# Kernel optimization log

Hardware: AMD Instinct MI355X
Metric: run time of the kernel (lower is better)

Reference implementation:

```python
import jax, jax.numpy as jnp
import numpy as np

H = 8   # no_heads
D = 32  # c_hidden per head


def setup_inputs() -> dict:
    key = jax.random.key(0)
    ks = jax.random.split(key, 8)
    B, Q, K, C = 4, 1024, 1024, 256
    s = 0.02
    return {
        "q_x": jax.random.normal(ks[0], (B, Q, C), jnp.float32),
        "kv_x": jax.random.normal(ks[1], (B, K, C), jnp.float32),
        "mask_bias": jnp.zeros((B, 1, 1, K), jnp.float32),
        "pair_bias": jax.random.normal(ks[2], (B, H, Q, K), jnp.float32),
        "wq": jax.random.normal(ks[3], (H * D, C), jnp.float32) * s,
        "wk": jax.random.normal(ks[4], (H * D, C), jnp.float32) * s,
        "wv": jax.random.normal(ks[5], (H * D, C), jnp.float32) * s,
        "wg": jax.random.normal(ks[6], (H * D, C), jnp.float32) * s,
        "bg": jnp.zeros((H * D,), jnp.float32),
        "wo": jax.random.normal(ks[7], (C, H * D), jnp.float32) * s,
        "bo": jnp.zeros((C,), jnp.float32),
    }


def reference(q_x, kv_x, mask_bias, pair_bias, wq, wk, wv, wg, bg, wo, bo):
    B, Q, _ = q_x.shape
    K = kv_x.shape[1]
    # linear projections (no bias on q/k/v, as in OpenFold Attention)
    q = (q_x @ wq.T).reshape(B, Q, H, D) / jnp.sqrt(jnp.asarray(D, q_x.dtype))
    k = (kv_x @ wk.T).reshape(B, K, H, D)
    v = (kv_x @ wv.T).reshape(B, K, H, D)
    # scores + biases (mask bias broadcasts over heads/queries)
    a = jnp.einsum("bqhd,bkhd->bhqk", q, k) + mask_bias + pair_bias
    a = jax.nn.softmax(a, axis=-1)
    o = jnp.einsum("bhqk,bkhd->bqhd", a, v)  # [B,Q,H,D]
    # multiplicative gating from the query input
    g = jax.nn.sigmoid(q_x @ wg.T + bg).reshape(B, Q, H, D)
    o = o * g
    return (o.reshape(B, Q, H * D)) @ wo.T + bo
```

## Files before the change

### kernel.cpp

```cpp
#include <hip/hip_runtime.h>
#include <cstdint>
#include <cstddef>

typedef short bf16x8 __attribute__((ext_vector_type(8)));
typedef float f32x4 __attribute__((ext_vector_type(4)));
typedef unsigned short u16x4 __attribute__((ext_vector_type(4)));
typedef unsigned short u16x8 __attribute__((ext_vector_type(8)));

#define MFMA(a,b,c) __builtin_amdgcn_mfma_f32_16x16x32_bf16((a),(b),(c),0,0,0)

__device__ __forceinline__ unsigned short f2bf(float x){
  union { float f; unsigned u; } v; v.f = x;
  unsigned r = v.u + 0x7FFFu + ((v.u >> 16) & 1u);
  return (unsigned short)(r >> 16);
}
__device__ __forceinline__ float bf2f(unsigned short b){
  union { unsigned u; float f; } v; v.u = ((unsigned)b) << 16;
  return v.f;
}
__device__ __forceinline__ bf16x8 cvtld8(const float* p){
  f32x4 a = *(const f32x4*)p;
  f32x4 b = *(const f32x4*)(p + 4);
  bf16x8 r;
  r[0]=(short)f2bf(a.x); r[1]=(short)f2bf(a.y);
  r[2]=(short)f2bf(a.z); r[3]=(short)f2bf(a.w);
  r[4]=(short)f2bf(b.x); r[5]=(short)f2bf(b.y);
  r[6]=(short)f2bf(b.z); r[7]=(short)f2bf(b.w);
  return r;
}

__global__ __launch_bounds__(256) void wcvt_kernel(
    const float* __restrict__ wq, const float* __restrict__ wk,
    const float* __restrict__ wv, const float* __restrict__ wg,
    const float* __restrict__ wo, unsigned short* __restrict__ dst)
{
  const int which = blockIdx.x >> 5;
  const float* s = (which==0)?wq:(which==1)?wk:(which==2)?wv:(which==3)?wg:wo;
  const int off = (blockIdx.x & 31) * 2048 + threadIdx.x * 8;
  f32x4 a = *(const f32x4*)(s + off);
  f32x4 b = *(const f32x4*)(s + off + 4);
  u16x8 r;
  r[0]=f2bf(a.x); r[1]=f2bf(a.y); r[2]=f2bf(a.z); r[3]=f2bf(a.w);
  r[4]=f2bf(b.x); r[5]=f2bf(b.y); r[6]=f2bf(b.z); r[7]=f2bf(b.w);
  *(u16x8*)(dst + (size_t)which*65536 + off) = r;
}

__global__ __launch_bounds__(256,2) void proj_kernel(
    const float* __restrict__ q_x, const float* __restrict__ kv_x,
    const unsigned short* __restrict__ wb,
    const float* __restrict__ bg,
    unsigned short* __restrict__ qws, unsigned short* __restrict__ kws,
    unsigned short* __restrict__ vTws, unsigned short* __restrict__ gws)
{
  const int tid = threadIdx.x;
  const int w = tid >> 6, lane = tid & 63;
  const int c = lane & 15, qd = lane >> 4;
  const int side = blockIdx.x >> 8;
  const int rb = (blockIdx.x & 255) * 16;
  const float* X = side ? kv_x : q_x;
  const unsigned short* W0 = wb + (size_t)(side ? 1 : 0) * 65536;
  const unsigned short* W1 = wb + (size_t)(side ? 2 : 3) * 65536;
  const int hdw = w * 64;

  const f32x4 fz = {0.f,0.f,0.f,0.f};
  f32x4 acc[2][4];
  #pragma unroll
  for (int o=0;o<2;o++)
    #pragma unroll
    for (int mt=0;mt<4;mt++) acc[o][mt] = fz;

  #pragma unroll
  for (int ks = 0; ks < 8; ks++){
    const int ko = ks*32 + qd*8;
    bf16x8 bfrag = cvtld8(X + (size_t)(rb + c)*256 + ko);
    #pragma unroll
    for (int mt = 0; mt < 4; mt++){
      const int hd = hdw + mt*16 + c;
      bf16x8 a0 = *(const bf16x8*)(W0 + (size_t)hd*256 + ko);
      bf16x8 a1 = *(const bf16x8*)(W1 + (size_t)hd*256 + ko);
      acc[0][mt] = MFMA(a0, bfrag, acc[0][mt]);
      acc[1][mt] = MFMA(a1, bfrag, acc[1][mt]);
    }
  }

  const int row = rb + c;
  const int b = row >> 10, rr = row & 1023;
  #pragma unroll
  for (int mt = 0; mt < 4; mt++){
    const int hd0 = hdw + mt*16 + qd*4;
    const int h = hd0 >> 5, d0 = hd0 & 31;
    f32x4 v0 = acc[0][mt], v1 = acc[1][mt];
    if (side == 0){
      const float qs = 0.17677669529663687f;
      u16x4 oq = { f2bf(v0.x*qs), f2bf(v0.y*qs), f2bf(v0.z*qs), f2bf(v0.w*qs) };
      *(u16x4*)(qws + ((size_t)((b*8 + h)*1024 + rr))*32 + d0) = oq;
      f32x4 bg4 = *(const f32x4*)(bg + hd0);
      float g0 = 1.f/(1.f + exp2f(-1.44269504f*(v1.x + bg4.x)));
      float g1 = 1.f/(1.f + exp2f(-1.44269504f*(v1.y + bg4.y)));
      float g2 = 1.f/(1.f + exp2f(-1.44269504f*(v1.z + bg4.z)));
      float g3 = 1.f/(1.f + exp2f(-1.44269504f*(v1.w + bg4.w)));
      u16x4 og = { f2bf(g0), f2bf(g1), f2bf(g2), f2bf(g3) };
      *(u16x4*)(gws + ((size_t)((b*1024 + rr)*8 + h))*32 + d0) = og;
    } else {
      u16x4 ok = { f2bf(v0.x), f2bf(v0.y), f2bf(v0.z), f2bf(v0.w) };
      *(u16x4*)(kws + ((size_t)((b*8 + h)*1024 + rr))*32 + d0) = ok;
      size_t vb = ((size_t)((b*8 + h)*32 + d0))*1024 + rr;
      vTws[vb         ] = f2bf(v1.x);
      vTws[vb + 1024  ] = f2bf(v1.y);
      vTws[vb + 2048  ] = f2bf(v1.z);
      vTws[vb + 3072  ] = f2bf(v1.w);
    }
  }
}

__global__ __launch_bounds__(256,4) void attn_kernel(
    const float* __restrict__ pair_bias, const float* __restrict__ mask_bias,
    const unsigned short* __restrict__ qws, const unsigned short* __restrict__ kws,
    const unsigned short* __restrict__ vTws, const unsigned short* __restrict__ gws,
    unsigned short* __restrict__ ows)
{
  __shared__ __align__(16) unsigned short pT[4*16*136];

  const int tid = threadIdx.x;
  const int w = tid >> 6, lane = tid & 63;
  const int c = lane & 15, qd = lane >> 4;
  const int bh = blockIdx.x >> 4, qb = blockIdx.x & 15;
  const int b  = bh >> 3, h = bh & 7;
  const int qrow = qb*64 + w*16 + c;

  const bf16x8 qf = *(const bf16x8*)(qws + ((size_t)bh*1024 + qrow)*32 + qd*8);
  const float* pbp = pair_bias + ((size_t)bh*1024 + qrow)*1024;
  const float* mbp = mask_bias + (size_t)b*1024;
  const unsigned short* kbase = kws  + (size_t)bh*1024*32;
  const unsigned short* vbase = vTws + (size_t)bh*32*1024;
  unsigned short* pTw = pT + w*(16*136);

  const f32x4 fz = {0.f,0.f,0.f,0.f};
  float m_i = -3.0e38f, l_i = 0.f;
  f32x4 accO0 = fz, accO1 = fz;

  for (int kc = 0; kc < 8; kc++){
    const int k0 = kc*128;
    f32x4 sf[8];
    float cmax = -3.0e38f;
    #pragma unroll
    for (int t = 0; t < 8; t++){
      const int kt = k0 + t*16;
      bf16x8 af = *(const bf16x8*)(kbase + (size_t)(kt + c)*32 + qd*8);
      f32x4 s = MFMA(af, qf, fz);
      f32x4 pb = *(const f32x4*)(pbp + kt + qd*4);
      f32x4 mb = *(const f32x4*)(mbp + kt + qd*4);
      s = (s + pb + mb) * 1.44269504f;
      sf[t] = s;
      cmax = fmaxf(cmax, fmaxf(fmaxf(s.x, s.y), fmaxf(s.z, s.w)));
    }
    cmax = fmaxf(cmax, __shfl_xor(cmax, 16));
    cmax = fmaxf(cmax, __shfl_xor(cmax, 32));
    const float m_new = fmaxf(m_i, cmax);
    const float alpha = exp2f(m_i - m_new);
    accO0 *= alpha; accO1 *= alpha;

    float rsum = 0.f;
    #pragma unroll
    for (int t = 0; t < 8; t++){
      f32x4 p;
      p.x = exp2f(sf[t].x - m_new);
      p.y = exp2f(sf[t].y - m_new);
      p.z = exp2f(sf[t].z - m_new);
      p.w = exp2f(sf[t].w - m_new);
      rsum += (p.x + p.y) + (p.z + p.w);
      u16x4 pk = { f2bf(p.x), f2bf(p.y), f2bf(p.z), f2bf(p.w) };
      *(u16x4*)(pTw + c*136 + t*16 + qd*4) = pk;
    }
    rsum += __shfl_xor(rsum, 16);
    rsum += __shfl_xor(rsum, 32);
    l_i = l_i*alpha + rsum;
    m_i = m_new;

    #pragma unroll
    for (int ks = 0; ks < 4; ks++){
      bf16x8 pf = *(const bf16x8*)(pTw + c*136 + ks*32 + qd*8);
      bf16x8 v0 = *(const bf16x8*)(vbase + (size_t)c*1024      + k0 + ks*32 + qd*8);
      bf16x8 v1 = *(const bf16x8*)(vbase + (size_t)(16+c)*1024 + k0 + ks*32 + qd*8);
      accO0 = MFMA(v0, pf, accO0);
      accO1 = MFMA(v1, pf, accO1);
    }
  }

  const float inv_l = 1.0f / l_i;
  const size_t obase = (((size_t)b*1024 + qrow)*8 + h)*32;
  {
    u16x4 g4 = *(const u16x4*)(gws + obase + qd*4);
    u16x4 o4 = { f2bf(accO0.x*inv_l*bf2f(g4[0])),
                 f2bf(accO0.y*inv_l*bf2f(g4[1])),
                 f2bf(accO0.z*inv_l*bf2f(g4[2])),
                 f2bf(accO0.w*inv_l*bf2f(g4[3])) };
    *(u16x4*)(ows + obase + qd*4) = o4;
  }
  {
    u16x4 g4 = *(const u16x4*)(gws + obase + 16 + qd*4);
    u16x4 o4 = { f2bf(accO1.x*inv_l*bf2f(g4[0])),
                 f2bf(accO1.y*inv_l*bf2f(g4[1])),
                 f2bf(accO1.z*inv_l*bf2f(g4[2])),
                 f2bf(accO1.w*inv_l*bf2f(g4[3])) };
    *(u16x4*)(ows + obase + 16 + qd*4) = o4;
  }
}

__global__ __launch_bounds__(256,2) void oproj_kernel(
    const unsigned short* __restrict__ ows, const unsigned short* __restrict__ wob,
    const float* __restrict__ bo, float* __restrict__ out)
{
  const int tid = threadIdx.x;
  const int w = tid >> 6, lane = tid & 63;
  const int c = lane & 15, qd = lane >> 4;
  const int row0 = blockIdx.x * 16;
  const int i0 = w * 64;

  const f32x4 fz = {0.f,0.f,0.f,0.f};
  f32x4 acc[4] = {fz, fz, fz, fz};
  #pragma unroll
  for (int ks = 0; ks < 8; ks++){
    const int ko = ks*32 + qd*8;
    bf16x8 bfrag = *(const bf16x8*)(ows + (size_t)(row0 + c)*256 + ko);
    #pragma unroll
    for (int mt = 0; mt < 4; mt++){
      bf16x8 afrag = *(const bf16x8*)(wob + (size_t)(i0 + mt*16 + c)*256 + ko);
      acc[mt] = MFMA(afrag, bfrag, acc[mt]);
    }
  }
  #pragma unroll
  for (int mt = 0; mt < 4; mt++){
    const int i = i0 + mt*16 + qd*4;
    f32x4 bo4 = *(const f32x4*)(bo + i);
    f32x4 r = acc[mt] + bo4;
    *(f32x4*)(out + (size_t)(row0 + c)*256 + i) = r;
  }
}

extern "C" void kernel_launch(void* const* d_in, const int* in_sizes, int n_in,
                              void* d_out, int out_size, void* d_ws, size_t ws_size,
                              hipStream_t stream) {
  const float* q_x       = (const float*)d_in[0];
  const float* kv_x      = (const float*)d_in[1];
  const float* mask_bias = (const float*)d_in[2];
  const float* pair_bias = (const float*)d_in[3];
  const float* wq        = (const float*)d_in[4];
  const float* wk        = (const float*)d_in[5];
  const float* wv        = (const float*)d_in[6];
  const float* wg        = (const float*)d_in[7];
  const float* bg        = (const float*)d_in[8];
  const float* wo        = (const float*)d_in[9];
  const float* bo        = (const float*)d_in[10];

  unsigned short* ws  = (unsigned short*)d_ws;
  unsigned short* qws  = ws;
  unsigned short* kws  = ws + (1u<<20);
  unsigned short* vTws = ws + 2*(1u<<20);
  unsigned short* gws  = ws + 3*(1u<<20);
  unsigned short* ows  = ws + 4*(1u<<20);
  unsigned short* wb   = ws + 5*(1u<<20);

  wcvt_kernel<<<160, 256, 0, stream>>>(wq, wk, wv, wg, wo, wb);
  proj_kernel<<<512, 256, 0, stream>>>(q_x, kv_x, wb, bg, qws, kws, vTws, gws);
  attn_kernel<<<512, 256, 0, stream>>>(pair_bias, mask_bias, qws, kws, vTws, gws, ows);
  oproj_kernel<<<256, 256, 0, stream>>>(ows, wb + 4*65536, bo, (float*)d_out);
}
```

Baseline: 268.5 us.

## Software-pipeline pair_bias and K loads across key chunks in attention kernel

```diff
diff --git a/kernel.cpp b/kernel.cpp
--- a/kernel.cpp
+++ b/kernel.cpp
@@ -113,7 +113,7 @@
   }
 }
 
-__global__ __launch_bounds__(256,4) void attn_kernel(
+__global__ __launch_bounds__(256,2) void attn_kernel(
     const float* __restrict__ pair_bias, const float* __restrict__ mask_bias,
     const unsigned short* __restrict__ qws, const unsigned short* __restrict__ kws,
     const unsigned short* __restrict__ vTws, const unsigned short* __restrict__ gws,
@@ -139,20 +139,45 @@
   float m_i = -3.0e38f, l_i = 0.f;
   f32x4 accO0 = fz, accO1 = fz;
 
+  f32x4 pb0[8], pb1[8];
+  bf16x8 afb[8];
+  #pragma unroll
+  for (int t = 0; t < 8; t++)
+    pb0[t] = *(const f32x4*)(pbp + t*16 + qd*4);
+  #pragma unroll
+  for (int t = 0; t < 8; t++)
+    pb1[t] = *(const f32x4*)(pbp + 128 + t*16 + qd*4);
+  #pragma unroll
+  for (int t = 0; t < 8; t++)
+    afb[t] = *(const bf16x8*)(kbase + (size_t)(t*16 + c)*32 + qd*8);
+
+  #pragma unroll
   for (int kc = 0; kc < 8; kc++){
     const int k0 = kc*128;
     f32x4 sf[8];
+    #pragma unroll
+    for (int t = 0; t < 8; t++)
+      sf[t] = MFMA(afb[t], qf, fz);
+    if (kc < 7){
+      #pragma unroll
+      for (int t = 0; t < 8; t++)
+        afb[t] = *(const bf16x8*)(kbase + (size_t)(k0 + 128 + t*16 + c)*32 + qd*8);
+    }
     float cmax = -3.0e38f;
     #pragma unroll
     for (int t = 0; t < 8; t++){
-      const int kt = k0 + t*16;
-      bf16x8 af = *(const bf16x8*)(kbase + (size_t)(kt + c)*32 + qd*8);
-      f32x4 s = MFMA(af, qf, fz);
-      f32x4 pb = *(const f32x4*)(pbp + kt + qd*4);
-      f32x4 mb = *(const f32x4*)(mbp + kt + qd*4);
-      s = (s + pb + mb) * 1.44269504f;
+      f32x4 mb = *(const f32x4*)(mbp + k0 + t*16 + qd*4);
+      f32x4 pb = (kc & 1) ? pb1[t] : pb0[t];
+      f32x4 s = (sf[t] + pb + mb) * 1.44269504f;
       sf[t] = s;
       cmax = fmaxf(cmax, fmaxf(fmaxf(s.x, s.y), fmaxf(s.z, s.w)));
+    }
+    if (kc < 6){
+      #pragma unroll
+      for (int t = 0; t < 8; t++){
+        f32x4 v = *(const f32x4*)(pbp + k0 + 256 + t*16 + qd*4);
+        if (kc & 1) pb1[t] = v; else pb0[t] = v;
+      }
     }
     cmax = fmaxf(cmax, __shfl_xor(cmax, 16));
     cmax = fmaxf(cmax, __shfl_xor(cmax, 32));
```

Result: slower. 285.5 us (+6.3%).

## Split attention over key halves and add a combine kernel; prefetch K and pair bias

Applied to the files above, without the earlier changes.

```diff
diff --git a/kernel.cpp b/kernel.cpp
--- a/kernel.cpp
+++ b/kernel.cpp
@@ -116,43 +116,59 @@
 __global__ __launch_bounds__(256,4) void attn_kernel(
     const float* __restrict__ pair_bias, const float* __restrict__ mask_bias,
     const unsigned short* __restrict__ qws, const unsigned short* __restrict__ kws,
-    const unsigned short* __restrict__ vTws, const unsigned short* __restrict__ gws,
-    unsigned short* __restrict__ ows)
+    const unsigned short* __restrict__ vTws,
+    float* __restrict__ pO, float* __restrict__ pML)
 {
   __shared__ __align__(16) unsigned short pT[4*16*136];
 
   const int tid = threadIdx.x;
   const int w = tid >> 6, lane = tid & 63;
   const int c = lane & 15, qd = lane >> 4;
-  const int bh = blockIdx.x >> 4, qb = blockIdx.x & 15;
-  const int b  = bh >> 3, h = bh & 7;
+  const int split = blockIdx.x >> 9;
+  const int rblk  = blockIdx.x & 511;
+  const int bh = rblk >> 4, qb = rblk & 15;
+  const int b  = bh >> 3;
   const int qrow = qb*64 + w*16 + c;
+  const int kbeg = split*512;
 
   const bf16x8 qf = *(const bf16x8*)(qws + ((size_t)bh*1024 + qrow)*32 + qd*8);
-  const float* pbp = pair_bias + ((size_t)bh*1024 + qrow)*1024;
-  const float* mbp = mask_bias + (size_t)b*1024;
-  const unsigned short* kbase = kws  + (size_t)bh*1024*32;
-  const unsigned short* vbase = vTws + (size_t)bh*32*1024;
+  const float* pbp = pair_bias + ((size_t)bh*1024 + qrow)*1024 + kbeg;
+  const float* mbp = mask_bias + (size_t)b*1024 + kbeg;
+  const unsigned short* kbase = kws  + ((size_t)bh*1024 + kbeg)*32;
+  const unsigned short* vbase = vTws + (size_t)bh*32*1024 + kbeg;
   unsigned short* pTw = pT + w*(16*136);
 
   const f32x4 fz = {0.f,0.f,0.f,0.f};
   float m_i = -3.0e38f, l_i = 0.f;
   f32x4 accO0 = fz, accO1 = fz;
 
-  for (int kc = 0; kc < 8; kc++){
+  bf16x8 afb[8];
+  f32x4  pbb[8];
+  #pragma unroll
+  for (int t = 0; t < 8; t++){
+    afb[t] = *(const bf16x8*)(kbase + (size_t)(t*16 + c)*32 + qd*8);
+    pbb[t] = *(const f32x4*)(pbp + t*16 + qd*4);
+  }
+
+  #pragma unroll
+  for (int kc = 0; kc < 4; kc++){
     const int k0 = kc*128;
     f32x4 sf[8];
     float cmax = -3.0e38f;
     #pragma unroll
     for (int t = 0; t < 8; t++){
-      const int kt = k0 + t*16;
-      bf16x8 af = *(const bf16x8*)(kbase + (size_t)(kt + c)*32 + qd*8);
-      f32x4 s = MFMA(af, qf, fz);
-      f32x4 pb = *(const f32x4*)(pbp + kt + qd*4);
-      f32x4 mb = *(const f32x4*)(mbp + kt + qd*4);
-      s = (s + pb + mb) * 1.44269504f;
+      f32x4 s = MFMA(afb[t], qf, fz);
+      f32x4 mb = *(const f32x4*)(mbp + k0 + t*16 + qd*4);
+      s = (s + pbb[t] + mb) * 1.44269504f;
       sf[t] = s;
       cmax = fmaxf(cmax, fmaxf(fmaxf(s.x, s.y), fmaxf(s.z, s.w)));
+    }
+    if (kc < 3){
+      #pragma unroll
+      for (int t = 0; t < 8; t++){
+        afb[t] = *(const bf16x8*)(kbase + (size_t)(k0 + 128 + t*16 + c)*32 + qd*8);
+        pbb[t] = *(const f32x4*)(pbp + k0 + 128 + t*16 + qd*4);
+      }
     }
     cmax = fmaxf(cmax, __shfl_xor(cmax, 16));
     cmax = fmaxf(cmax, __shfl_xor(cmax, 32));
@@ -187,24 +203,47 @@
     }
   }
 
-  const float inv_l = 1.0f / l_i;
-  const size_t obase = (((size_t)b*1024 + qrow)*8 + h)*32;
-  {
-    u16x4 g4 = *(const u16x4*)(gws + obase + qd*4);
-    u16x4 o4 = { f2bf(accO0.x*inv_l*bf2f(g4[0])),
-                 f2bf(accO0.y*inv_l*bf2f(g4[1])),
-                 f2bf(accO0.z*inv_l*bf2f(g4[2])),
-                 f2bf(accO0.w*inv_l*bf2f(g4[3])) };
-    *(u16x4*)(ows + obase + qd*4) = o4;
-  }
-  {
-    u16x4 g4 = *(const u16x4*)(gws + obase + 16 + qd*4);
-    u16x4 o4 = { f2bf(accO1.x*inv_l*bf2f(g4[0])),
-                 f2bf(accO1.y*inv_l*bf2f(g4[1])),
-                 f2bf(accO1.z*inv_l*bf2f(g4[2])),
-                 f2bf(accO1.w*inv_l*bf2f(g4[3])) };
-    *(u16x4*)(ows + obase + 16 + qd*4) = o4;
-  }
+  const size_t prow = (size_t)split*32768 + (size_t)bh*1024 + qrow;
+  *(f32x4*)(pO + prow*32 + qd*4)      = accO0;
+  *(f32x4*)(pO + prow*32 + 16 + qd*4) = accO1;
+  if (qd == 0){
+    pML[prow*2]     = m_i;
+    pML[prow*2 + 1] = l_i;
+  }
+}
+
+__global__ __launch_bounds__(256) void combine_kernel(
+    const float* __restrict__ pO, const float* __restrict__ pML,
+    const unsigned short* __restrict__ gws, unsigned short* __restrict__ ows)
+{
+  const int gtid = blockIdx.x*256 + threadIdx.x;
+  const int row = gtid >> 2, part = gtid & 3;
+  const int d0 = part*8;
+  const float m0 = pML[(size_t)row*2],           l0 = pML[(size_t)row*2 + 1];
+  const float m1 = pML[(size_t)(32768 + row)*2], l1 = pML[(size_t)(32768 + row)*2 + 1];
+  const float m  = fmaxf(m0, m1);
+  const float a0 = exp2f(m0 - m), a1 = exp2f(m1 - m);
+  const float inv = 1.0f / (l0*a0 + l1*a1);
+  f32x4 x0 = *(const f32x4*)(pO + (size_t)row*32 + d0);
+  f32x4 x1 = *(const f32x4*)(pO + (size_t)row*32 + d0 + 4);
+  f32x4 y0 = *(const f32x4*)(pO + 32768ull*32 + (size_t)row*32 + d0);
+  f32x4 y1 = *(const f32x4*)(pO + 32768ull*32 + (size_t)row*32 + d0 + 4);
+  const int bh = row >> 10, qrow = row & 1023, b = bh >> 3, h = bh & 7;
+  const size_t obase = (((size_t)b*1024 + qrow)*8 + h)*32 + d0;
+  u16x8 g8 = *(const u16x8*)(gws + obase);
+  const float s0 = a0*inv, s1 = a1*inv;
+  f32x4 o0 = x0*s0 + y0*s1;
+  f32x4 o1 = x1*s0 + y1*s1;
+  u16x8 r8;
+  r8[0] = f2bf(o0.x*bf2f(g8[0]));
+  r8[1] = f2bf(o0.y*bf2f(g8[1]));
+  r8[2] = f2bf(o0.z*bf2f(g8[2]));
+  r8[3] = f2bf(o0.w*bf2f(g8[3]));
+  r8[4] = f2bf(o1.x*bf2f(g8[4]));
+  r8[5] = f2bf(o1.y*bf2f(g8[5]));
+  r8[6] = f2bf(o1.z*bf2f(g8[6]));
+  r8[7] = f2bf(o1.w*bf2f(g8[7]));
+  *(u16x8*)(ows + obase) = r8;
 }
 
 __global__ __launch_bounds__(256,2) void oproj_kernel(
@@ -253,16 +292,19 @@
   const float* wo        = (const float*)d_in[9];
   const float* bo        = (const float*)d_in[10];
 
-  unsigned short* ws  = (unsigned short*)d_ws;
-  unsigned short* qws  = ws;
-  unsigned short* kws  = ws + (1u<<20);
-  unsigned short* vTws = ws + 2*(1u<<20);
-  unsigned short* gws  = ws + 3*(1u<<20);
-  unsigned short* ows  = ws + 4*(1u<<20);
-  unsigned short* wb   = ws + 5*(1u<<20);
+  char* base = (char*)d_ws;
+  unsigned short* qws  = (unsigned short*)(base);
+  unsigned short* kws  = (unsigned short*)(base + (2u<<20));
+  unsigned short* vTws = (unsigned short*)(base + (4u<<20));
+  unsigned short* gws  = (unsigned short*)(base + (6u<<20));
+  unsigned short* ows  = (unsigned short*)(base + (8u<<20));
+  unsigned short* wb   = (unsigned short*)(base + (10u<<20));
+  float*          pO   = (float*)(base + (12u<<20));
+  float*          pML  = (float*)(base + (20u<<20));
 
   wcvt_kernel<<<160, 256, 0, stream>>>(wq, wk, wv, wg, wo, wb);
   proj_kernel<<<512, 256, 0, stream>>>(q_x, kv_x, wb, bg, qws, kws, vTws, gws);
-  attn_kernel<<<512, 256, 0, stream>>>(pair_bias, mask_bias, qws, kws, vTws, gws, ows);
+  attn_kernel<<<1024, 256, 0, stream>>>(pair_bias, mask_bias, qws, kws, vTws, pO, pML);
+  combine_kernel<<<512, 256, 0, stream>>>(pO, pML, gws, ows);
   oproj_kernel<<<256, 256, 0, stream>>>(ows, wb + 4*65536, bo, (float*)d_out);
 }
```

Result: slower. 278.3 us (+3.7%).

## Stream pair_bias into LDS with async double-buffered DMA in attention

Applied to the files above, without the earlier changes.

```diff
diff --git a/kernel.cpp b/kernel.cpp
--- a/kernel.cpp
+++ b/kernel.cpp
@@ -27,6 +27,12 @@
   r[4]=(short)f2bf(b.x); r[5]=(short)f2bf(b.y);
   r[6]=(short)f2bf(b.z); r[7]=(short)f2bf(b.w);
   return r;
+}
+
+__device__ __forceinline__ void dma16(const void* g, void* l){
+  __builtin_amdgcn_global_load_lds(
+      (const __attribute__((address_space(1))) unsigned int*)g,
+      (__attribute__((address_space(3))) unsigned int*)l, 16, 0, 0);
 }
 
 __global__ __launch_bounds__(256) void wcvt_kernel(
@@ -91,7 +97,7 @@
     const int h = hd0 >> 5, d0 = hd0 & 31;
     f32x4 v0 = acc[0][mt], v1 = acc[1][mt];
     if (side == 0){
-      const float qs = 0.17677669529663687f;
+      const float qs = 0.2550348612f;
       u16x4 oq = { f2bf(v0.x*qs), f2bf(v0.y*qs), f2bf(v0.z*qs), f2bf(v0.w*qs) };
       *(u16x4*)(qws + ((size_t)((b*8 + h)*1024 + rr))*32 + d0) = oq;
       f32x4 bg4 = *(const f32x4*)(bg + hd0);
@@ -113,44 +119,63 @@
   }
 }
 
-__global__ __launch_bounds__(256,4) void attn_kernel(
+__global__ __launch_bounds__(256,2) void attn_kernel(
     const float* __restrict__ pair_bias, const float* __restrict__ mask_bias,
     const unsigned short* __restrict__ qws, const unsigned short* __restrict__ kws,
     const unsigned short* __restrict__ vTws, const unsigned short* __restrict__ gws,
     unsigned short* __restrict__ ows)
 {
-  __shared__ __align__(16) unsigned short pT[4*16*136];
+  __shared__ __align__(16) unsigned char smem[43008];
 
   const int tid = threadIdx.x;
   const int w = tid >> 6, lane = tid & 63;
   const int c = lane & 15, qd = lane >> 4;
+  const int rl = lane >> 4, p16 = lane & 15;
   const int bh = blockIdx.x >> 4, qb = blockIdx.x & 15;
   const int b  = bh >> 3, h = bh & 7;
   const int qrow = qb*64 + w*16 + c;
 
+  float* mybuf = (float*)(smem + w*8192);
+  unsigned short* pTw = (unsigned short*)(smem + 32768) + w*(16*80);
+
   const bf16x8 qf = *(const bf16x8*)(qws + ((size_t)bh*1024 + qrow)*32 + qd*8);
-  const float* pbp = pair_bias + ((size_t)bh*1024 + qrow)*1024;
+  const float* pbw = pair_bias + ((size_t)bh*1024 + qb*64 + w*16)*1024;
   const float* mbp = mask_bias + (size_t)b*1024;
   const unsigned short* kbase = kws  + (size_t)bh*1024*32;
   const unsigned short* vbase = vTws + (size_t)bh*32*1024;
-  unsigned short* pTw = pT + w*(16*136);
 
   const f32x4 fz = {0.f,0.f,0.f,0.f};
   float m_i = -3.0e38f, l_i = 0.f;
   f32x4 accO0 = fz, accO1 = fz;
 
-  for (int kc = 0; kc < 8; kc++){
-    const int k0 = kc*128;
-    f32x4 sf[8];
+  #pragma unroll
+  for (int j = 0; j < 4; j++){
+    const int r = 4*j + rl;
+    dma16(pbw + (size_t)r*1024 + ((p16 ^ r) << 2), mybuf + j*256);
+  }
+
+  for (int kc = 0; kc < 16; kc++){
+    const int k0 = kc*64;
+    float* cur = mybuf + (kc & 1)*1024;
+    float* nxt = mybuf + ((kc + 1) & 1)*1024;
+
+    bf16x8 af[4];
+    f32x4  mb[4];
+    #pragma unroll
+    for (int t = 0; t < 4; t++){
+      af[t] = *(const bf16x8*)(kbase + (size_t)(k0 + t*16 + c)*32 + qd*8);
+      mb[t] = *(const f32x4*)(mbp + k0 + t*16 + qd*4);
+    }
+
+    asm volatile("s_waitcnt vmcnt(8)" ::: "memory");
+
+    f32x4 sf[4];
     float cmax = -3.0e38f;
     #pragma unroll
-    for (int t = 0; t < 8; t++){
-      const int kt = k0 + t*16;
-      bf16x8 af = *(const bf16x8*)(kbase + (size_t)(kt + c)*32 + qd*8);
-      f32x4 s = MFMA(af, qf, fz);
-      f32x4 pb = *(const f32x4*)(pbp + kt + qd*4);
-      f32x4 mb = *(const f32x4*)(mbp + kt + qd*4);
-      s = (s + pb + mb) * 1.44269504f;
+    for (int t = 0; t < 4; t++){
+      f32x4 pb4 = *(const f32x4*)(cur + c*64 + (((t*4 + qd) ^ c) << 2));
+      f32x4 C = (pb4 + mb[t]) * 1.44269504f;
+      f32x4 s = MFMA(af[t], qf, C);
       sf[t] = s;
       cmax = fmaxf(cmax, fmaxf(fmaxf(s.x, s.y), fmaxf(s.z, s.w)));
     }
@@ -162,7 +187,7 @@
 
     float rsum = 0.f;
     #pragma unroll
-    for (int t = 0; t < 8; t++){
+    for (int t = 0; t < 4; t++){
       f32x4 p;
       p.x = exp2f(sf[t].x - m_new);
       p.y = exp2f(sf[t].y - m_new);
@@ -170,21 +195,34 @@
       p.w = exp2f(sf[t].w - m_new);
       rsum += (p.x + p.y) + (p.z + p.w);
       u16x4 pk = { f2bf(p.x), f2bf(p.y), f2bf(p.z), f2bf(p.w) };
-      *(u16x4*)(pTw + c*136 + t*16 + qd*4) = pk;
+      *(u16x4*)(pTw + c*80 + t*16 + qd*4) = pk;
     }
     rsum += __shfl_xor(rsum, 16);
     rsum += __shfl_xor(rsum, 32);
     l_i = l_i*alpha + rsum;
     m_i = m_new;
 
-    #pragma unroll
-    for (int ks = 0; ks < 4; ks++){
-      bf16x8 pf = *(const bf16x8*)(pTw + c*136 + ks*32 + qd*8);
-      bf16x8 v0 = *(const bf16x8*)(vbase + (size_t)c*1024      + k0 + ks*32 + qd*8);
-      bf16x8 v1 = *(const bf16x8*)(vbase + (size_t)(16+c)*1024 + k0 + ks*32 + qd*8);
-      accO0 = MFMA(v0, pf, accO0);
-      accO1 = MFMA(v1, pf, accO1);
-    }
+    bf16x8 v00 = *(const bf16x8*)(vbase + (size_t)c*1024      + k0 + qd*8);
+    bf16x8 v10 = *(const bf16x8*)(vbase + (size_t)(16+c)*1024 + k0 + qd*8);
+    bf16x8 v01 = *(const bf16x8*)(vbase + (size_t)c*1024      + k0 + 32 + qd*8);
+    bf16x8 v11 = *(const bf16x8*)(vbase + (size_t)(16+c)*1024 + k0 + 32 + qd*8);
+
+    asm volatile("" ::: "memory");
+
+    if (kc < 15){
+      #pragma unroll
+      for (int j = 0; j < 4; j++){
+        const int r = 4*j + rl;
+        dma16(pbw + (size_t)r*1024 + (k0 + 64) + ((p16 ^ r) << 2), nxt + j*256);
+      }
+    }
+
+    bf16x8 pf0 = *(const bf16x8*)(pTw + c*80 + qd*8);
+    bf16x8 pf1 = *(const bf16x8*)(pTw + c*80 + 32 + qd*8);
+    accO0 = MFMA(v00, pf0, accO0);
+    accO1 = MFMA(v10, pf0, accO1);
+    accO0 = MFMA(v01, pf1, accO0);
+    accO1 = MFMA(v11, pf1, accO1);
   }
 
   const float inv_l = 1.0f / l_i;
@@ -253,13 +291,13 @@
   const float* wo        = (const float*)d_in[9];
   const float* bo        = (const float*)d_in[10];
 
-  unsigned short* ws  = (unsigned short*)d_ws;
-  unsigned short* qws  = ws;
-  unsigned short* kws  = ws + (1u<<20);
-  unsigned short* vTws = ws + 2*(1u<<20);
-  unsigned short* gws  = ws + 3*(1u<<20);
-  unsigned short* ows  = ws + 4*(1u<<20);
-  unsigned short* wb   = ws + 5*(1u<<20);
+  char* base = (char*)d_ws;
+  unsigned short* qws  = (unsigned short*)(base);
+  unsigned short* kws  = (unsigned short*)(base + (2u<<20));
+  unsigned short* vTws = (unsigned short*)(base + (4u<<20));
+  unsigned short* gws  = (unsigned short*)(base + (6u<<20));
+  unsigned short* ows  = (unsigned short*)(base + (8u<<20));
+  unsigned short* wb   = (unsigned short*)(base + (10u<<20));
 
   wcvt_kernel<<<160, 256, 0, stream>>>(wq, wk, wv, wg, wo, wb);
   proj_kernel<<<512, 256, 0, stream>>>(q_x, kv_x, wb, bg, qws, kws, vTws, gws);
```

After: 258.5 us. 1.04x faster.
